# Performance work log

Hardware: AMD Instinct MI355X
Metric: run time of the kernel (lower is better)

## Reference

```python
import jax, jax.numpy as jnp
import numpy as np

B, A, H1, H2 = 128, 64, 256, 256


def setup_inputs() -> dict:
    key = jax.random.key(0)
    k1, k2, k3, k4, k5, k6 = jax.random.split(key, 6)
    scale = 0.01
    return {
        "userAspRep": jax.random.normal(k1, (B, A, H1), dtype=jnp.float32),
        "itemAspRep": jax.random.normal(k2, (B, A, H1), dtype=jnp.float32),
        "W_u": jax.random.uniform(k3, (H2, H1), jnp.float32, -scale, scale),
        "W_i": jax.random.uniform(k4, (H2, H1), jnp.float32, -scale, scale),
        "w_hu": jax.random.uniform(k5, (H2, 1), jnp.float32, -scale, scale),
        "w_hi": jax.random.uniform(k6, (H2, 1), jnp.float32, -scale, scale),
    }


def reference(userAspRep, itemAspRep, W_u, W_i, w_hu, w_hi):
    # L1 pairwise similarity: sim[b,u,i] = 1 / (1 + sum_h |U[b,u,h] - I[b,i,h]|)
    diff = jnp.abs(userAspRep[:, :, None, :] - itemAspRep[:, None, :, :])  # [B,Au,Ai,H1]
    sim = 1.0 / (1.0 + diff.sum(axis=-1))  # [B,Au,Ai]

    Wu_u = jnp.einsum('kh,buh->bku', W_u, userAspRep)  # [B,H2,Au]
    Wi_i = jnp.einsum('kh,bih->bki', W_i, itemAspRep)  # [B,H2,Ai]

    # User aspect importance
    H_u = jax.nn.relu(Wu_u + jnp.einsum('bki,bui->bku', Wi_i, sim))  # [B,H2,Au]
    user_scores = jnp.einsum('k,bku->bu', w_hu[:, 0], H_u)  # [B,Au]
    userAspImpt = jax.nn.softmax(user_scores, axis=1)

    # Item aspect importance
    H_i = jax.nn.relu(Wi_i + jnp.einsum('bku,bui->bki', Wu_u, sim))  # [B,H2,Ai]
    item_scores = jnp.einsum('k,bki->bi', w_hi[:, 0], H_i)  # [B,Ai]
    itemAspImpt = jax.nn.softmax(item_scores, axis=1)

    return (userAspImpt, itemAspImpt)
```

## Files before the change

### kernel.cpp

```cpp
#include <hip/hip_runtime.h>

#define NB 128
#define NA 64
#define NH1 256
#define NH2 256

typedef __attribute__((ext_vector_type(8))) short bf16x8;
typedef __attribute__((ext_vector_type(4))) float f32x4;
typedef __attribute__((ext_vector_type(8))) unsigned short u16x8;
typedef __attribute__((ext_vector_type(4))) unsigned short u16x4;
typedef _Float16 f16x2 __attribute__((ext_vector_type(2)));

__device__ __forceinline__ unsigned short f2bf(float f) {
    union { float f; unsigned u; } v; v.f = f;
    unsigned r = v.u + 0x7FFFu + ((v.u >> 16) & 1u);
    return (unsigned short)(r >> 16);
}
__device__ __forceinline__ f16x2 habs2(f16x2 x) {
    union { f16x2 h; unsigned u; } v; v.h = x; v.u &= 0x7FFF7FFFu; return v.h;
}

#define XSWZ(row, cb) ((cb) ^ (((row) & 7) << 4))

__global__ __launch_bounds__(256) void cvt_w(
    const float* __restrict__ Wu, const float* __restrict__ Wi,
    unsigned short* __restrict__ Wub, unsigned short* __restrict__ Wib)
{
    const size_t e = ((size_t)blockIdx.x * 256 + threadIdx.x) * 8;
    const float* src; unsigned short* dst; size_t off;
    if (e < 65536) { src = Wu; dst = Wub; off = e; }
    else           { src = Wi; dst = Wib; off = e - 65536; }
    float4 a = *reinterpret_cast<const float4*>(src + off);
    float4 b = *reinterpret_cast<const float4*>(src + off + 4);
    u16x8 o;
    o[0] = f2bf(a.x); o[1] = f2bf(a.y); o[2] = f2bf(a.z); o[3] = f2bf(a.w);
    o[4] = f2bf(b.x); o[5] = f2bf(b.y); o[6] = f2bf(b.z); o[7] = f2bf(b.w);
    *reinterpret_cast<u16x8*>(dst + off) = o;
}

#define SROW 264
__global__ __launch_bounds__(512) void sim_kernel(
    const float* __restrict__ U, const float* __restrict__ I,
    unsigned short* __restrict__ SIM, unsigned short* __restrict__ SIMT)
{
    __shared__ __align__(16) _Float16 sh[96 * SROW];
    const int t = threadIdx.x, b = blockIdx.x, uh = blockIdx.y;

    const float4* Ug = reinterpret_cast<const float4*>(U + ((size_t)b * NA + uh * 32) * NH1);
    const float4* Ig = reinterpret_cast<const float4*>(I + (size_t)b * NA * NH1);
    #pragma unroll
    for (int it = 0; it < 12; ++it) {
        const int g = t + it * 512;
        float4 v = (g < 2048) ? Ug[g] : Ig[g - 2048];
        const int row = g >> 6, c4 = g & 63;
        f16x2 h0; h0.x = (_Float16)v.x; h0.y = (_Float16)v.y;
        f16x2 h1; h1.x = (_Float16)v.z; h1.y = (_Float16)v.w;
        union { f16x2 h[2]; float2 f; } pk; pk.h[0] = h0; pk.h[1] = h1;
        *reinterpret_cast<float2*>(&sh[row * SROW + c4 * 4]) = pk.f;
    }
    __syncthreads();

    const int tx = t & 15, ty = t >> 4;
    f16x2 acc[4];
    #pragma unroll
    for (int di = 0; di < 4; ++di) { acc[di].x = (_Float16)0; acc[di].y = (_Float16)0; }

    const _Float16* Urow = &sh[ty * SROW];
    #pragma unroll 4
    for (int h8 = 0; h8 < 32; ++h8) {
        union { float4 f; f16x2 h[4]; } uv, iv;
        uv.f = *reinterpret_cast<const float4*>(&Urow[h8 * 8]);
        #pragma unroll
        for (int di = 0; di < 4; ++di) {
            iv.f = *reinterpret_cast<const float4*>(&sh[(32 + tx + di * 16) * SROW + h8 * 8]);
            #pragma unroll
            for (int c = 0; c < 4; ++c)
                acc[di] = acc[di] + habs2(uv.h[c] - iv.h[c]);
        }
    }

    const int u = uh * 32 + ty;
    unsigned short* SB = SIM  + (size_t)b * NA * NA;
    unsigned short* TB = SIMT + (size_t)b * NA * NA;
    #pragma unroll
    for (int di = 0; di < 4; ++di) {
        const int i = tx + di * 16;
        const float sum = (float)acc[di].x + (float)acc[di].y;
        const unsigned short sv = f2bf(1.0f / (1.0f + sum));
        SB[(size_t)u * NA + i] = sv;
        TB[(size_t)i * NA + u] = sv;
    }
}

__global__ __launch_bounds__(512) void fused_kernel(
    const float* __restrict__ U, const float* __restrict__ I,
    const unsigned short* __restrict__ Wub, const unsigned short* __restrict__ Wib,
    const unsigned short* __restrict__ SIM, const unsigned short* __restrict__ SIMT,
    const float* __restrict__ whu, const float* __restrict__ whi,
    float* __restrict__ out)
{
    __shared__ __align__(16) unsigned short Xl[2 * 64 * 256];
    __shared__ __align__(16) unsigned short Pl[256 * 64];
    __shared__ float red[8 * 64];
    const int t = threadIdx.x, b = blockIdx.x, s = blockIdx.y;

    #pragma unroll
    for (int it = 0; it < 16; ++it) {
        const int g = t + it * 512;
        const int side = g >> 12, rem = g & 4095;
        const int row = rem >> 6, c4 = rem & 63;
        const float* X = side ? I : U;
        float4 v = *reinterpret_cast<const float4*>(X + ((size_t)b * NA + row) * NH1 + c4 * 4);
        u16x4 o;
        o[0] = f2bf(v.x); o[1] = f2bf(v.y); o[2] = f2bf(v.z); o[3] = f2bf(v.w);
        char* dst = (char*)Xl + side * 32768 + row * 512 + XSWZ(row, c4 * 8);
        *reinterpret_cast<u16x4*>(dst) = o;
    }
    __syncthreads();

    const int w  = __builtin_amdgcn_readfirstlane(t >> 6);
    const int l  = t & 63;
    const int lr = l & 15;
    const int lk = (l >> 4) * 8;

    const unsigned short* Ws = s ? Wib : Wub;
    const unsigned short* Wo = s ? Wub : Wib;

    f32x4 accO[2][4], accX[2][4];
    #pragma unroll
    for (int kt = 0; kt < 2; ++kt)
        #pragma unroll
        for (int at = 0; at < 4; ++at) { accO[kt][at] = (f32x4)(0.f); accX[kt][at] = (f32x4)(0.f); }

    #pragma unroll
    for (int h0 = 0; h0 < NH1; h0 += 32) {
        bf16x8 as_[2], ao_[2], bs_[4], bo_[4];
        #pragma unroll
        for (int kt = 0; kt < 2; ++kt) {
            const size_t roff = (size_t)(w * 32 + kt * 16 + lr) * NH1 + h0 + lk;
            as_[kt] = *reinterpret_cast<const bf16x8*>(Ws + roff);
            ao_[kt] = *reinterpret_cast<const bf16x8*>(Wo + roff);
        }
        #pragma unroll
        for (int at = 0; at < 4; ++at) {
            const int row = at * 16 + lr;
            const int cb  = XSWZ(row, (h0 + lk) * 2);
            bs_[at] = *reinterpret_cast<const bf16x8*>((char*)Xl + s * 32768 + row * 512 + cb);
            bo_[at] = *reinterpret_cast<const bf16x8*>((char*)Xl + (s ^ 1) * 32768 + row * 512 + cb);
        }
        #pragma unroll
        for (int kt = 0; kt < 2; ++kt)
            #pragma unroll
            for (int at = 0; at < 4; ++at) {
                accO[kt][at] = __builtin_amdgcn_mfma_f32_16x16x32_bf16(as_[kt], bs_[at], accO[kt][at], 0, 0, 0);
                accX[kt][at] = __builtin_amdgcn_mfma_f32_16x16x32_bf16(ao_[kt], bo_[at], accX[kt][at], 0, 0, 0);
            }
    }

    #pragma unroll
    for (int kt = 0; kt < 2; ++kt) {
        const int kb = w * 32 + kt * 16 + (l >> 4) * 4;
        #pragma unroll
        for (int at = 0; at < 4; ++at)
            #pragma unroll
            for (int r = 0; r < 4; ++r) {
                const int row = kb + r;
                *reinterpret_cast<unsigned short*>(
                    (char*)Pl + row * 128 + XSWZ(row, (at * 16 + lr) * 2)) = f2bf(accX[kt][at][r]);
            }
    }
    __syncthreads();

    const unsigned short* SMg = (s ? SIMT : SIM) + (size_t)b * NA * NA;
    const float* wv = s ? whi : whu;

    bf16x8 bfr2[2][4];
    #pragma unroll
    for (int kk2 = 0; kk2 < 2; ++kk2)
        #pragma unroll
        for (int ot = 0; ot < 4; ++ot)
            bfr2[kk2][ot] = *reinterpret_cast<const bf16x8*>(
                SMg + (size_t)(ot * 16 + lr) * NA + kk2 * 32 + lk);

    float partial[4] = {0.f, 0.f, 0.f, 0.f};
    #pragma unroll
    for (int kt = 0; kt < 2; ++kt) {
        f32x4 sacc[4];
        #pragma unroll
        for (int ot = 0; ot < 4; ++ot) sacc[ot] = (f32x4)(0.f);
        #pragma unroll
        for (int kk2 = 0; kk2 < 2; ++kk2) {
            const int arow = w * 32 + kt * 16 + lr;
            bf16x8 af = *reinterpret_cast<const bf16x8*>(
                (char*)Pl + arow * 128 + XSWZ(arow, (kk2 * 32 + lk) * 2));
            #pragma unroll
            for (int ot = 0; ot < 4; ++ot)
                sacc[ot] = __builtin_amdgcn_mfma_f32_16x16x32_bf16(af, bfr2[kk2][ot], sacc[ot], 0, 0, 0);
        }
        const int kb = w * 32 + kt * 16 + (l >> 4) * 4;
        float wr[4];
        #pragma unroll
        for (int r = 0; r < 4; ++r) wr[r] = wv[kb + r];
        #pragma unroll
        for (int ot = 0; ot < 4; ++ot) {
            float p = 0.f;
            #pragma unroll
            for (int r = 0; r < 4; ++r) {
                float h = accO[kt][ot][r] + sacc[ot][r];
                h = fmaxf(h, 0.f);
                p = fmaf(wr[r], h, p);
            }
            partial[ot] += p;
        }
    }
    #pragma unroll
    for (int ot = 0; ot < 4; ++ot) {
        partial[ot] += __shfl_xor(partial[ot], 16, 64);
        partial[ot] += __shfl_xor(partial[ot], 32, 64);
    }
    if (l < 16) {
        #pragma unroll
        for (int ot = 0; ot < 4; ++ot) red[w * 64 + ot * 16 + l] = partial[ot];
    }
    __syncthreads();

    if (t < 64) {
        float sc = 0.f;
        #pragma unroll
        for (int q = 0; q < 8; ++q) sc += red[q * 64 + t];
        float m = sc;
        #pragma unroll
        for (int off = 32; off >= 1; off >>= 1) m = fmaxf(m, __shfl_xor(m, off, 64));
        float e = __expf(sc - m);
        float ssum = e;
        #pragma unroll
        for (int off = 32; off >= 1; off >>= 1) ssum += __shfl_xor(ssum, off, 64);
        out[(size_t)s * (NB * NA) + (size_t)b * NA + t] = e / ssum;
    }
}

extern "C" void kernel_launch(void* const* d_in, const int* in_sizes, int n_in,
                              void* d_out, int out_size, void* d_ws, size_t ws_size,
                              hipStream_t stream)
{
    (void)in_sizes; (void)n_in; (void)out_size; (void)ws_size;
    const float* U   = (const float*)d_in[0];
    const float* I   = (const float*)d_in[1];
    const float* Wu  = (const float*)d_in[2];
    const float* Wi  = (const float*)d_in[3];
    const float* whu = (const float*)d_in[4];
    const float* whi = (const float*)d_in[5];
    float* out = (float*)d_out;

    char* ws = (char*)d_ws;
    unsigned short* Wub   = (unsigned short*)(ws);
    unsigned short* Wib   = (unsigned short*)(ws + 131072);
    unsigned short* SIMb  = (unsigned short*)(ws + 262144);
    unsigned short* SIMTb = (unsigned short*)(ws + 1310720);

    cvt_w<<<64, 256, 0, stream>>>(Wu, Wi, Wub, Wib);
    sim_kernel<<<dim3(NB, 2), 512, 0, stream>>>(U, I, SIMb, SIMTb);
    fused_kernel<<<dim3(NB, 2), 512, 0, stream>>>(U, I, Wub, Wib, SIMb, SIMTb, whu, whi, out);
}
```

Before: 94.96 us.

## Fold weight conversion into sim kernel and double threads per block

Removes the separate cvt_w launch by having the first 512 threads of each sim block convert one slice of the W matrices to bf16 (256 blocks x 512 = 131072 elements). Both sim_kernel and fused_kernel now run 1024 threads per block. In sim_kernel the H dimension is split in half across thread pairs and combined with a shuffle. In fused_kernel each wave owns 16 rows of H2 instead of 32, which halves the accumulator registers per thread. The aim is to save a launch and raise per-block parallelism, at the cost of scalar, uncoalesced-width conversion stores and a larger reduction buffer.

```diff
diff --git a/kernel.cpp b/kernel.cpp
--- a/kernel.cpp
+++ b/kernel.cpp
@@ -22,35 +22,28 @@
 
 #define XSWZ(row, cb) ((cb) ^ (((row) & 7) << 4))
 
-__global__ __launch_bounds__(256) void cvt_w(
+#define SROW 264
+__global__ __launch_bounds__(1024) void sim_kernel(
+    const float* __restrict__ U, const float* __restrict__ I,
     const float* __restrict__ Wu, const float* __restrict__ Wi,
-    unsigned short* __restrict__ Wub, unsigned short* __restrict__ Wib)
-{
-    const size_t e = ((size_t)blockIdx.x * 256 + threadIdx.x) * 8;
-    const float* src; unsigned short* dst; size_t off;
-    if (e < 65536) { src = Wu; dst = Wub; off = e; }
-    else           { src = Wi; dst = Wib; off = e - 65536; }
-    float4 a = *reinterpret_cast<const float4*>(src + off);
-    float4 b = *reinterpret_cast<const float4*>(src + off + 4);
-    u16x8 o;
-    o[0] = f2bf(a.x); o[1] = f2bf(a.y); o[2] = f2bf(a.z); o[3] = f2bf(a.w);
-    o[4] = f2bf(b.x); o[5] = f2bf(b.y); o[6] = f2bf(b.z); o[7] = f2bf(b.w);
-    *reinterpret_cast<u16x8*>(dst + off) = o;
-}
-
-#define SROW 264
-__global__ __launch_bounds__(512) void sim_kernel(
-    const float* __restrict__ U, const float* __restrict__ I,
+    unsigned short* __restrict__ Wub, unsigned short* __restrict__ Wib,
     unsigned short* __restrict__ SIM, unsigned short* __restrict__ SIMT)
 {
     __shared__ __align__(16) _Float16 sh[96 * SROW];
     const int t = threadIdx.x, b = blockIdx.x, uh = blockIdx.y;
 
+    if (t < 512) {
+        const int bl = b * 2 + uh;
+        const int e = bl * 512 + t;
+        if (e < 65536) Wub[e] = f2bf(Wu[e]);
+        else           Wib[e - 65536] = f2bf(Wi[e - 65536]);
+    }
+
     const float4* Ug = reinterpret_cast<const float4*>(U + ((size_t)b * NA + uh * 32) * NH1);
     const float4* Ig = reinterpret_cast<const float4*>(I + (size_t)b * NA * NH1);
     #pragma unroll
-    for (int it = 0; it < 12; ++it) {
-        const int g = t + it * 512;
+    for (int it = 0; it < 6; ++it) {
+        const int g = t + it * 1024;
         float4 v = (g < 2048) ? Ug[g] : Ig[g - 2048];
         const int row = g >> 6, c4 = g & 63;
         f16x2 h0; h0.x = (_Float16)v.x; h0.y = (_Float16)v.y;
@@ -60,39 +53,49 @@
     }
     __syncthreads();
 
-    const int tx = t & 15, ty = t >> 4;
+    const int tx = t & 15;
+    const int hh = (t >> 4) & 1;
+    const int ty = t >> 5;
     f16x2 acc[4];
     #pragma unroll
     for (int di = 0; di < 4; ++di) { acc[di].x = (_Float16)0; acc[di].y = (_Float16)0; }
 
-    const _Float16* Urow = &sh[ty * SROW];
+    const _Float16* Urow = &sh[ty * SROW + hh * 128];
     #pragma unroll 4
-    for (int h8 = 0; h8 < 32; ++h8) {
+    for (int h8 = 0; h8 < 16; ++h8) {
         union { float4 f; f16x2 h[4]; } uv, iv;
         uv.f = *reinterpret_cast<const float4*>(&Urow[h8 * 8]);
         #pragma unroll
         for (int di = 0; di < 4; ++di) {
-            iv.f = *reinterpret_cast<const float4*>(&sh[(32 + tx + di * 16) * SROW + h8 * 8]);
+            iv.f = *reinterpret_cast<const float4*>(
+                &sh[(32 + tx + di * 16) * SROW + hh * 128 + h8 * 8]);
             #pragma unroll
             for (int c = 0; c < 4; ++c)
                 acc[di] = acc[di] + habs2(uv.h[c] - iv.h[c]);
         }
     }
 
-    const int u = uh * 32 + ty;
-    unsigned short* SB = SIM  + (size_t)b * NA * NA;
-    unsigned short* TB = SIMT + (size_t)b * NA * NA;
+    float s[4];
     #pragma unroll
     for (int di = 0; di < 4; ++di) {
-        const int i = tx + di * 16;
-        const float sum = (float)acc[di].x + (float)acc[di].y;
-        const unsigned short sv = f2bf(1.0f / (1.0f + sum));
-        SB[(size_t)u * NA + i] = sv;
-        TB[(size_t)i * NA + u] = sv;
-    }
-}
-
-__global__ __launch_bounds__(512) void fused_kernel(
+        s[di] = (float)acc[di].x + (float)acc[di].y;
+        s[di] += __shfl_xor(s[di], 16, 64);
+    }
+    if (hh == 0) {
+        const int u = uh * 32 + ty;
+        unsigned short* SB = SIM  + (size_t)b * NA * NA;
+        unsigned short* TB = SIMT + (size_t)b * NA * NA;
+        #pragma unroll
+        for (int di = 0; di < 4; ++di) {
+            const int i = tx + di * 16;
+            const unsigned short sv = f2bf(1.0f / (1.0f + s[di]));
+            SB[(size_t)u * NA + i] = sv;
+            TB[(size_t)i * NA + u] = sv;
+        }
+    }
+}
+
+__global__ __launch_bounds__(1024) void fused_kernel(
     const float* __restrict__ U, const float* __restrict__ I,
     const unsigned short* __restrict__ Wub, const unsigned short* __restrict__ Wib,
     const unsigned short* __restrict__ SIM, const unsigned short* __restrict__ SIMT,
@@ -101,12 +104,12 @@
 {
     __shared__ __align__(16) unsigned short Xl[2 * 64 * 256];
     __shared__ __align__(16) unsigned short Pl[256 * 64];
-    __shared__ float red[8 * 64];
+    __shared__ float red[16 * 64];
     const int t = threadIdx.x, b = blockIdx.x, s = blockIdx.y;
 
     #pragma unroll
-    for (int it = 0; it < 16; ++it) {
-        const int g = t + it * 512;
+    for (int it = 0; it < 8; ++it) {
+        const int g = t + it * 1024;
         const int side = g >> 12, rem = g & 4095;
         const int row = rem >> 6, c4 = rem & 63;
         const float* X = side ? I : U;
@@ -122,25 +125,21 @@
     const int l  = t & 63;
     const int lr = l & 15;
     const int lk = (l >> 4) * 8;
+    const int k0 = w * 16;
 
     const unsigned short* Ws = s ? Wib : Wub;
     const unsigned short* Wo = s ? Wub : Wib;
 
-    f32x4 accO[2][4], accX[2][4];
-    #pragma unroll
-    for (int kt = 0; kt < 2; ++kt)
-        #pragma unroll
-        for (int at = 0; at < 4; ++at) { accO[kt][at] = (f32x4)(0.f); accX[kt][at] = (f32x4)(0.f); }
+    f32x4 accO[4], accX[4];
+    #pragma unroll
+    for (int at = 0; at < 4; ++at) { accO[at] = (f32x4)(0.f); accX[at] = (f32x4)(0.f); }
 
     #pragma unroll
     for (int h0 = 0; h0 < NH1; h0 += 32) {
-        bf16x8 as_[2], ao_[2], bs_[4], bo_[4];
-        #pragma unroll
-        for (int kt = 0; kt < 2; ++kt) {
-            const size_t roff = (size_t)(w * 32 + kt * 16 + lr) * NH1 + h0 + lk;
-            as_[kt] = *reinterpret_cast<const bf16x8*>(Ws + roff);
-            ao_[kt] = *reinterpret_cast<const bf16x8*>(Wo + roff);
-        }
+        bf16x8 as_, ao_, bs_[4], bo_[4];
+        const size_t roff = (size_t)(k0 + lr) * NH1 + h0 + lk;
+        as_ = *reinterpret_cast<const bf16x8*>(Ws + roff);
+        ao_ = *reinterpret_cast<const bf16x8*>(Wo + roff);
         #pragma unroll
         for (int at = 0; at < 4; ++at) {
             const int row = at * 16 + lr;
@@ -149,24 +148,21 @@
             bo_[at] = *reinterpret_cast<const bf16x8*>((char*)Xl + (s ^ 1) * 32768 + row * 512 + cb);
         }
         #pragma unroll
-        for (int kt = 0; kt < 2; ++kt)
-            #pragma unroll
-            for (int at = 0; at < 4; ++at) {
-                accO[kt][at] = __builtin_amdgcn_mfma_f32_16x16x32_bf16(as_[kt], bs_[at], accO[kt][at], 0, 0, 0);
-                accX[kt][at] = __builtin_amdgcn_mfma_f32_16x16x32_bf16(ao_[kt], bo_[at], accX[kt][at], 0, 0, 0);
-            }
-    }
-
-    #pragma unroll
-    for (int kt = 0; kt < 2; ++kt) {
-        const int kb = w * 32 + kt * 16 + (l >> 4) * 4;
+        for (int at = 0; at < 4; ++at) {
+            accO[at] = __builtin_amdgcn_mfma_f32_16x16x32_bf16(as_, bs_[at], accO[at], 0, 0, 0);
+            accX[at] = __builtin_amdgcn_mfma_f32_16x16x32_bf16(ao_, bo_[at], accX[at], 0, 0, 0);
+        }
+    }
+
+    {
+        const int kb = k0 + (l >> 4) * 4;
         #pragma unroll
         for (int at = 0; at < 4; ++at)
             #pragma unroll
             for (int r = 0; r < 4; ++r) {
                 const int row = kb + r;
                 *reinterpret_cast<unsigned short*>(
-                    (char*)Pl + row * 128 + XSWZ(row, (at * 16 + lr) * 2)) = f2bf(accX[kt][at][r]);
+                    (char*)Pl + row * 128 + XSWZ(row, (at * 16 + lr) * 2)) = f2bf(accX[at][r]);
             }
     }
     __syncthreads();
@@ -174,44 +170,37 @@
     const unsigned short* SMg = (s ? SIMT : SIM) + (size_t)b * NA * NA;
     const float* wv = s ? whi : whu;
 
-    bf16x8 bfr2[2][4];
-    #pragma unroll
-    for (int kk2 = 0; kk2 < 2; ++kk2)
-        #pragma unroll
-        for (int ot = 0; ot < 4; ++ot)
-            bfr2[kk2][ot] = *reinterpret_cast<const bf16x8*>(
+    f32x4 sacc[4];
+    #pragma unroll
+    for (int ot = 0; ot < 4; ++ot) sacc[ot] = (f32x4)(0.f);
+    #pragma unroll
+    for (int kk2 = 0; kk2 < 2; ++kk2) {
+        const int arow = k0 + lr;
+        bf16x8 af = *reinterpret_cast<const bf16x8*>(
+            (char*)Pl + arow * 128 + XSWZ(arow, (kk2 * 32 + lk) * 2));
+        #pragma unroll
+        for (int ot = 0; ot < 4; ++ot) {
+            bf16x8 bf = *reinterpret_cast<const bf16x8*>(
                 SMg + (size_t)(ot * 16 + lr) * NA + kk2 * 32 + lk);
-
-    float partial[4] = {0.f, 0.f, 0.f, 0.f};
-    #pragma unroll
-    for (int kt = 0; kt < 2; ++kt) {
-        f32x4 sacc[4];
-        #pragma unroll
-        for (int ot = 0; ot < 4; ++ot) sacc[ot] = (f32x4)(0.f);
-        #pragma unroll
-        for (int kk2 = 0; kk2 < 2; ++kk2) {
-            const int arow = w * 32 + kt * 16 + lr;
-            bf16x8 af = *reinterpret_cast<const bf16x8*>(
-                (char*)Pl + arow * 128 + XSWZ(arow, (kk2 * 32 + lk) * 2));
-            #pragma unroll
-            for (int ot = 0; ot < 4; ++ot)
-                sacc[ot] = __builtin_amdgcn_mfma_f32_16x16x32_bf16(af, bfr2[kk2][ot], sacc[ot], 0, 0, 0);
-        }
-        const int kb = w * 32 + kt * 16 + (l >> 4) * 4;
-        float wr[4];
-        #pragma unroll
-        for (int r = 0; r < 4; ++r) wr[r] = wv[kb + r];
-        #pragma unroll
-        for (int ot = 0; ot < 4; ++ot) {
-            float p = 0.f;
-            #pragma unroll
-            for (int r = 0; r < 4; ++r) {
-                float h = accO[kt][ot][r] + sacc[ot][r];
-                h = fmaxf(h, 0.f);
-                p = fmaf(wr[r], h, p);
-            }
-            partial[ot] += p;
-        }
+            sacc[ot] = __builtin_amdgcn_mfma_f32_16x16x32_bf16(af, bf, sacc[ot], 0, 0, 0);
+        }
+    }
+
+    const int kb = k0 + (l >> 4) * 4;
+    float wr[4];
+    #pragma unroll
+    for (int r = 0; r < 4; ++r) wr[r] = wv[kb + r];
+    float partial[4];
+    #pragma unroll
+    for (int ot = 0; ot < 4; ++ot) {
+        float p = 0.f;
+        #pragma unroll
+        for (int r = 0; r < 4; ++r) {
+            float h = accO[ot][r] + sacc[ot][r];
+            h = fmaxf(h, 0.f);
+            p = fmaf(wr[r], h, p);
+        }
+        partial[ot] = p;
     }
     #pragma unroll
     for (int ot = 0; ot < 4; ++ot) {
@@ -227,7 +216,7 @@
     if (t < 64) {
         float sc = 0.f;
         #pragma unroll
-        for (int q = 0; q < 8; ++q) sc += red[q * 64 + t];
+        for (int q = 0; q < 16; ++q) sc += red[q * 64 + t];
         float m = sc;
         #pragma unroll
         for (int off = 32; off >= 1; off >>= 1) m = fmaxf(m, __shfl_xor(m, off, 64));
@@ -258,7 +247,6 @@
     unsigned short* SIMb  = (unsigned short*)(ws + 262144);
     unsigned short* SIMTb = (unsigned short*)(ws + 1310720);
 
-    cvt_w<<<64, 256, 0, stream>>>(Wu, Wi, Wub, Wib);
-    sim_kernel<<<dim3(NB, 2), 512, 0, stream>>>(U, I, SIMb, SIMTb);
-    fused_kernel<<<dim3(NB, 2), 512, 0, stream>>>(U, I, Wub, Wib, SIMb, SIMTb, whu, whi, out);
-}
+    sim_kernel<<<dim3(NB, 2), 1024, 0, stream>>>(U, I, Wu, Wi, Wub, Wib, SIMb, SIMTb);
+    fused_kernel<<<dim3(NB, 2), 1024, 0, stream>>>(U, I, Wub, Wib, SIMb, SIMTb, whu, whi, out);
+}
```

Result: slower. 97.86 us (+3.1%).
